# Kernel tuning notes

Measured on AMD Instinct MI355X. Metric: run time of the kernel, lower is better.

The kernel has to match this reference:

```python
import jax, jax.numpy as jnp
import numpy as np

N = 50000   # nodes
E = 100000  # directed edges
G = 2048    # graphs in batch
D = 32      # hidden dim
F_NODE = 11
F_EDGE = 4


def setup_inputs() -> dict:
    key = jax.random.key(0)
    ks = jax.random.split(key, 12)
    s = 0.1
    return {
        "x": jax.random.normal(ks[0], (N, F_NODE), dtype=jnp.float32),
        "edge_attr": jax.random.uniform(ks[1], (E, F_EDGE), dtype=jnp.float32),
        "lin0_w": jax.random.normal(ks[2], (D, F_NODE), dtype=jnp.float32) * s,
        "lin0_b": jnp.zeros((D,), jnp.float32),
        "nn_w": jax.random.normal(ks[3], (D * D, F_EDGE), dtype=jnp.float32) * s,
        "nn_b": jnp.zeros((D * D,), jnp.float32),
        "root_w": jax.random.normal(ks[4], (D, D), dtype=jnp.float32) * s,
        "conv_b": jnp.zeros((D,), jnp.float32),
        "gru_wi": jax.random.normal(ks[5], (3 * D, D), dtype=jnp.float32) * s,
        "gru_wh": jax.random.normal(ks[6], (3 * D, D), dtype=jnp.float32) * s,
        "gru_bi": jnp.zeros((3 * D,), jnp.float32),
        "gru_bh": jnp.zeros((3 * D,), jnp.float32),
        "lin1_w": jax.random.normal(ks[7], (2, D), dtype=jnp.float32) * s,
        "lin1_b": jnp.zeros((2,), jnp.float32),
        "edge_index": jax.random.randint(ks[8], (2, E), 0, N, dtype=jnp.int32),
        "batch": jnp.sort(jax.random.randint(ks[9], (N,), 0, G, dtype=jnp.int32)),
    }


def _gru_step(m, h, wi, wh, bi, bh):
    # single-step torch.nn.GRU cell math
    gi = m @ wi.T + bi            # [N, 3D]
    gh = h @ wh.T + bh            # [N, 3D]
    ir, iz, inn = jnp.split(gi, 3, axis=-1)
    hr, hz, hn = jnp.split(gh, 3, axis=-1)
    r = jax.nn.sigmoid(ir + hr)
    z = jax.nn.sigmoid(iz + hz)
    n = jnp.tanh(inn + r * hn)
    return (1.0 - z) * n + z * h


def reference(x, edge_attr, lin0_w, lin0_b, nn_w, nn_b, root_w, conv_b,
              gru_wi, gru_wh, gru_bi, gru_bh, lin1_w, lin1_b,
              edge_index, batch):
    src, dst = edge_index[0], edge_index[1]
    out = jax.nn.relu(x @ lin0_w.T + lin0_b)   # [N, D]
    h = out
    # per-edge 32x32 weight from edge MLP (edge_attr fixed -> hoisted out of loop)
    W_e = (edge_attr @ nn_w.T + nn_b).reshape(E, D, D)
    for _ in range(3):
        msg = jnp.einsum('ei,eio->eo', out[src], W_e)                  # [E, D]
        aggr = jax.ops.segment_sum(msg, dst, num_segments=N)           # add-aggregate
        m = jax.nn.relu(aggr + out @ root_w + conv_b)                  # NNConv root + bias
        h = _gru_step(m, h, gru_wi, gru_wh, gru_bi, gru_bh)
        out = h
    cnt = jax.ops.segment_sum(jnp.ones((N,), x.dtype), batch, num_segments=G)
    pooled = jax.ops.segment_sum(out, batch, num_segments=G) / jnp.maximum(cnt, 1.0)[:, None]
    logits = pooled @ lin1_w.T + lin1_b                                # [G, 2]
    return jax.nn.log_softmax(logits, axis=1)
```

## Files before the change

### kernel.cpp

```cpp
#include <hip/hip_runtime.h>
#include <hip/hip_bf16.h>

#define NN 50000
#define EE 100000
#define GG 2048
#define NB2 391

typedef float v2f __attribute__((ext_vector_type(2)));
__device__ __forceinline__ v2f fma2(v2f a, float b, v2f c) {
    return __builtin_elementwise_fma(a, (v2f){b, b}, c);
}

__device__ __forceinline__ float b2f(unsigned short u) {
    union { unsigned int i; float f; } x; x.i = (unsigned int)u << 16; return x.f;
}
__device__ __forceinline__ unsigned short f2b(float f) {
    union { float f; unsigned int i; } x; x.f = f;
    unsigned int b = x.i + (0x7FFFu + ((x.i >> 16) & 1u));
    return (unsigned short)(b >> 16);
}

__global__ __launch_bounds__(256) void k_setup(
    const float* __restrict__ x, const float* __restrict__ lw,
    const float* __restrict__ lb, const float* __restrict__ nnw,
    const float* __restrict__ nnb, const float* __restrict__ rootw,
    const float* __restrict__ wi, const float* __restrict__ wh,
    const int* __restrict__ ei, float* __restrict__ feat,
    float* __restrict__ Wre, float4* __restrict__ rw4,
    float4* __restrict__ wi4, int* __restrict__ cnt) {
    int blk = blockIdx.x;
    int t = threadIdx.x;
    if (blk < 6250) {
        int idx = blk * 256 + t;
        if (idx >= NN * 32) return;
        int n = idx >> 5, o = idx & 31;
        const float* xr = x + n * 11;
        const float* wr = lw + o * 11;
        float acc = lb[o];
#pragma unroll
        for (int i = 0; i < 11; ++i) acc += xr[i] * wr[i];
        feat[idx] = fmaxf(acc, 0.f);
    } else if (blk < 6278) {
        int idx = (blk - 6250) * 256 + t;
        if (idx < 5120) {
            int c = idx >> 5, i = idx & 31;
            float v;
            if (c < 128) v = nnw[((i << 5) + (c & 31)) * 4 + (c >> 5)];
            else         v = nnb[(i << 5) + (c - 128)];
            Wre[idx] = v;
        } else if (idx < 6144) {
            int j = idx - 5120;
            int k = j >> 5, o = j & 31;
            rw4[j] = make_float4(rootw[k * 32 + o], wh[o * 32 + k],
                                 wh[(32 + o) * 32 + k], wh[(64 + o) * 32 + k]);
        } else if (idx < 7168) {
            int j = idx - 6144;
            int k = j >> 5, o = j & 31;
            wi4[j] = make_float4(wi[o * 32 + k], wi[(32 + o) * 32 + k],
                                 wi[(64 + o) * 32 + k], 0.f);
        }
    } else {
        int e = (blk - 6278) * 256 + t;
        if (e >= EE) return;
        atomicAdd(&cnt[ei[EE + e]], 1);
        atomicAdd(&cnt[NN + ei[e]], 1);
    }
}

__global__ __launch_bounds__(256) void k_scan1(const int* __restrict__ cnt,
                                               int* __restrict__ tmp,
                                               int* __restrict__ bsum) {
    __shared__ int sd[256];
    int t = threadIdx.x;
    int i = blockIdx.x * 256 + t;
    int v = (i < 2 * NN) ? cnt[i] : 0;
    sd[t] = v;
    __syncthreads();
#pragma unroll
    for (int off = 1; off < 256; off <<= 1) {
        int x = (t >= off) ? sd[t - off] : 0;
        __syncthreads();
        sd[t] += x;
        __syncthreads();
    }
    if (i < 2 * NN) tmp[i] = sd[t];
    if (t == 255) bsum[blockIdx.x] = sd[255];
}

__global__ __launch_bounds__(512) void k_scan2(int* __restrict__ bsum) {
    __shared__ int sd[512];
    int t = threadIdx.x;
    int v = (t < NB2) ? bsum[t] : 0;
    sd[t] = v;
    __syncthreads();
#pragma unroll
    for (int off = 1; off < 512; off <<= 1) {
        int x = (t >= off) ? sd[t - off] : 0;
        __syncthreads();
        sd[t] += x;
        __syncthreads();
    }
    if (t < NB2) bsum[t] = sd[t];
}

__global__ void k_scan3(const int* __restrict__ cnt, const int* __restrict__ tmp,
                        const int* __restrict__ bsum, int* __restrict__ row_ptr,
                        int* __restrict__ cursor, int* __restrict__ out_ptr,
                        int* __restrict__ cursor2) {
    int i = blockIdx.x * blockDim.x + threadIdx.x;
    if (i >= 2 * NN) return;
    int base = (blockIdx.x > 0) ? bsum[blockIdx.x - 1] : 0;
    int excl = base + tmp[i] - cnt[i];
    if (i < NN) {
        row_ptr[i] = excl;
        cursor[i] = excl;
        if (i == 0) row_ptr[NN] = EE;
    } else {
        int j = i - NN;
        out_ptr[j] = excl - EE;
        cursor2[j] = excl - EE;
        if (j == 0) out_ptr[NN] = EE;
    }
}

__global__ __launch_bounds__(256) void k_scatter_y(
    const int* __restrict__ ei, const float* __restrict__ ea,
    int* __restrict__ cursor, int* __restrict__ cursor2,
    int* __restrict__ esrc, float4* __restrict__ eea,
    int* __restrict__ oslot, float4* __restrict__ oea,
    const float* __restrict__ feat, const float* __restrict__ Wre,
    unsigned short* __restrict__ yb) {
    int blk = blockIdx.x;
    if (blk < 391) {
        int e = blk * 256 + threadIdx.x;
        if (e >= EE) return;
        int s = ei[e], d = ei[EE + e];
        float4 a = make_float4(ea[e * 4 + 0], ea[e * 4 + 1], ea[e * 4 + 2], ea[e * 4 + 3]);
        int slot = atomicAdd(&cursor[d], 1);
        esrc[slot] = s;
        eea[slot] = a;
        int pos = atomicAdd(&cursor2[s], 1);
        oslot[pos] = slot;
        oea[pos] = a;
        return;
    }
    int by = blk - 391;
    int bx = by % 782, q = by / 782;
    int lane = threadIdx.x & 63;
    int wv = __builtin_amdgcn_readfirstlane(threadIdx.x >> 6);
    int n = bx * 64 + lane;
    if (n >= NN) return;
    int c0 = q * 40 + wv * 10;
    float fr[32];
    const float4* f4 = (const float4*)(feat + (long)n * 32);
#pragma unroll
    for (int qq = 0; qq < 8; ++qq) {
        float4 v = f4[qq];
        fr[4 * qq + 0] = v.x; fr[4 * qq + 1] = v.y;
        fr[4 * qq + 2] = v.z; fr[4 * qq + 3] = v.w;
    }
    float acc[10];
#pragma unroll
    for (int cc = 0; cc < 10; ++cc) {
        const float* w = Wre + (c0 + cc) * 32;
        float a = 0.f;
#pragma unroll
        for (int i = 0; i < 32; ++i) a += fr[i] * w[i];
        acc[cc] = a;
    }
    unsigned short* yr = yb + (long)n * 160 + c0;
#pragma unroll
    for (int qq = 0; qq < 5; ++qq) {
        unsigned int wlo = f2b(acc[2 * qq]);
        unsigned int whi = f2b(acc[2 * qq + 1]);
        ((unsigned int*)yr)[qq] = wlo | (whi << 16);
    }
}

__global__ __launch_bounds__(256) void k_msg(
    const unsigned short* __restrict__ yb, const int* __restrict__ esrc,
    const float4* __restrict__ eea, float* __restrict__ msg) {
    int idx = blockIdx.x * 256 + threadIdx.x;
    if (idx >= EE * 32) return;
    int slot = idx >> 5, o = idx & 31;
    int s = esrc[slot];
    float4 a = eea[slot];
    const unsigned short* yr = yb + (long)s * 160;
    float y0 = b2f(yr[o]);
    float y1 = b2f(yr[32 + o]);
    float y2 = b2f(yr[64 + o]);
    float y3 = b2f(yr[96 + o]);
    float y4 = b2f(yr[128 + o]);
    msg[idx] = y4 + a.x * y0 + a.y * y1 + a.z * y2 + a.w * y3;
}

__global__ __launch_bounds__(256) void k_conv_update(
    const float* __restrict__ msg_in, const int* __restrict__ row_ptr,
    const float4* __restrict__ rw4, const float* __restrict__ convb,
    const float4* __restrict__ wi4, const float* __restrict__ bi,
    const float* __restrict__ bh, const float4* __restrict__ nnw4,
    const float* __restrict__ nnb, const int* __restrict__ out_ptr,
    const int* __restrict__ oslot, const float4* __restrict__ oea,
    float* __restrict__ feat, float* __restrict__ msg_out, int write_msg) {
    __shared__ float fsT[32][36];
    __shared__ float msT[32][36];
    int t = threadIdx.x;
    int g = t >> 5, o = t & 31;
    int gc = g * 4;
    int nb = blockIdx.x * 32 + gc;
    float f[4], m[4];
    float cb = convb[o];
#pragma unroll
    for (int j = 0; j < 4; ++j) {
        int n = nb + j;
        bool v = (n < NN);
        f[j] = v ? feat[n * 32 + o] : 0.f;
        m[j] = cb;
        if (v) {
            int e0 = row_ptr[n], e1 = row_ptr[n + 1];
            for (int e = e0; e < e1; ++e)
                m[j] += msg_in[(e << 5) + o];
        }
    }
    *(float4*)&fsT[o][gc] = make_float4(f[0], f[1], f[2], f[3]);
    __syncthreads();

    float bhr = bh[o], bhz = bh[32 + o], bhn = bh[64 + o];
    v2f m01 = {m[0], m[1]}, m23 = {m[2], m[3]};
    v2f ghr01 = {bhr, bhr}, ghr23 = {bhr, bhr};
    v2f ghz01 = {bhz, bhz}, ghz23 = {bhz, bhz};
    v2f ghn01 = {bhn, bhn}, ghn23 = {bhn, bhn};
#pragma unroll 4
    for (int i = 0; i < 32; ++i) {
        float4 w = rw4[i * 32 + o];
        float4 fv = *(const float4*)&fsT[i][gc];
        v2f f01 = {fv.x, fv.y}, f23 = {fv.z, fv.w};
        m01 = fma2(f01, w.x, m01);   m23 = fma2(f23, w.x, m23);
        ghr01 = fma2(f01, w.y, ghr01); ghr23 = fma2(f23, w.y, ghr23);
        ghz01 = fma2(f01, w.z, ghz01); ghz23 = fma2(f23, w.z, ghz23);
        ghn01 = fma2(f01, w.w, ghn01); ghn23 = fma2(f23, w.w, ghn23);
    }
    float mm0 = fmaxf(m01.x, 0.f), mm1 = fmaxf(m01.y, 0.f);
    float mm2 = fmaxf(m23.x, 0.f), mm3 = fmaxf(m23.y, 0.f);
    *(float4*)&msT[o][gc] = make_float4(mm0, mm1, mm2, mm3);
    __syncthreads();

    float bir = bi[o], biz = bi[32 + o], bin_ = bi[64 + o];
    v2f gir01 = {bir, bir}, gir23 = {bir, bir};
    v2f giz01 = {biz, biz}, giz23 = {biz, biz};
    v2f gin01 = {bin_, bin_}, gin23 = {bin_, bin_};
#pragma unroll 4
    for (int k = 0; k < 32; ++k) {
        float4 w = wi4[k * 32 + o];
        float4 mv = *(const float4*)&msT[k][gc];
        v2f p01 = {mv.x, mv.y}, p23 = {mv.z, mv.w};
        gir01 = fma2(p01, w.x, gir01); gir23 = fma2(p23, w.x, gir23);
        giz01 = fma2(p01, w.y, giz01); giz23 = fma2(p23, w.y, giz23);
        gin01 = fma2(p01, w.z, gin01); gin23 = fma2(p23, w.z, gin23);
    }
    float girA[4] = {gir01.x, gir01.y, gir23.x, gir23.y};
    float gizA[4] = {giz01.x, giz01.y, giz23.x, giz23.y};
    float ginA[4] = {gin01.x, gin01.y, gin23.x, gin23.y};
    float ghrA[4] = {ghr01.x, ghr01.y, ghr23.x, ghr23.y};
    float ghzA[4] = {ghz01.x, ghz01.y, ghz23.x, ghz23.y};
    float ghnA[4] = {ghn01.x, ghn01.y, ghn23.x, ghn23.y};
    float fn[4];
#pragma unroll
    for (int j = 0; j < 4; ++j) {
        int n = nb + j;
        float r = 1.f / (1.f + __expf(-(girA[j] + ghrA[j])));
        float z = 1.f / (1.f + __expf(-(gizA[j] + ghzA[j])));
        float nt = tanhf(ginA[j] + r * ghnA[j]);
        fn[j] = (1.f - z) * nt + z * f[j];
        if (n < NN) feat[n * 32 + o] = fn[j];
    }
    if (!write_msg) return;

    *(float4*)&fsT[o][gc] = make_float4(fn[0], fn[1], fn[2], fn[3]);
    v2f y0_01 = {0.f, 0.f}, y0_23 = {0.f, 0.f};
    v2f y1_01 = {0.f, 0.f}, y1_23 = {0.f, 0.f};
    v2f y2_01 = {0.f, 0.f}, y2_23 = {0.f, 0.f};
    v2f y3_01 = {0.f, 0.f}, y3_23 = {0.f, 0.f};
    v2f y4_01 = {0.f, 0.f}, y4_23 = {0.f, 0.f};
#pragma unroll 4
    for (int i = 0; i < 32; ++i) {
        float4 w = nnw4[i * 32 + o];
        float w1 = nnb[i * 32 + o];
        float4 fv = *(const float4*)&fsT[i][gc];
        v2f f01 = {fv.x, fv.y}, f23 = {fv.z, fv.w};
        y0_01 = fma2(f01, w.x, y0_01); y0_23 = fma2(f23, w.x, y0_23);
        y1_01 = fma2(f01, w.y, y1_01); y1_23 = fma2(f23, w.y, y1_23);
        y2_01 = fma2(f01, w.z, y2_01); y2_23 = fma2(f23, w.z, y2_23);
        y3_01 = fma2(f01, w.w, y3_01); y3_23 = fma2(f23, w.w, y3_23);
        y4_01 = fma2(f01, w1, y4_01);  y4_23 = fma2(f23, w1, y4_23);
    }
    float ya0[4] = {y0_01.x, y0_01.y, y0_23.x, y0_23.y};
    float ya1[4] = {y1_01.x, y1_01.y, y1_23.x, y1_23.y};
    float ya2[4] = {y2_01.x, y2_01.y, y2_23.x, y2_23.y};
    float ya3[4] = {y3_01.x, y3_01.y, y3_23.x, y3_23.y};
    float ya4[4] = {y4_01.x, y4_01.y, y4_23.x, y4_23.y};
#pragma unroll
    for (int j = 0; j < 4; ++j) {
        int n = nb + j;
        if (n < NN) {
            int p0 = out_ptr[n], p1 = out_ptr[n + 1];
            for (int p = p0; p < p1; ++p) {
                float4 a = oea[p];
                int slot = oslot[p];
                msg_out[(slot << 5) + o] =
                    ya4[j] + a.x * ya0[j] + a.y * ya1[j]
                           + a.z * ya2[j] + a.w * ya3[j];
            }
        }
    }
}

__global__ __launch_bounds__(64) void k_pool_final(
    const float* __restrict__ feat, const int* __restrict__ batch,
    const float* __restrict__ w, const float* __restrict__ b,
    float* __restrict__ out) {
    int g = blockIdx.x;
    int t = threadIdx.x;
    int o = t & 31, h = t >> 5;
    int lo = 0, hi = NN;
    while (lo < hi) { int mid = (lo + hi) >> 1; if (batch[mid] < g) lo = mid + 1; else hi = mid; }
    int start = lo;
    hi = NN;
    while (lo < hi) { int mid = (lo + hi) >> 1; if (batch[mid] <= g) lo = mid + 1; else hi = mid; }
    int end = lo;
    float acc = 0.f;
    for (int n = start + h; n < end; n += 2) acc += feat[(long)n * 32 + o];
    acc += __shfl_xor(acc, 32, 64);
    float p = acc / fmaxf((float)(end - start), 1.f);
    float l0 = p * w[o], l1 = p * w[32 + o];
#pragma unroll
    for (int s = 16; s >= 1; s >>= 1) {
        l0 += __shfl_xor(l0, s, 64);
        l1 += __shfl_xor(l1, s, 64);
    }
    if (t == 0) {
        l0 += b[0]; l1 += b[1];
        float mx = fmaxf(l0, l1);
        float lse = mx + logf(__expf(l0 - mx) + __expf(l1 - mx));
        out[g * 2 + 0] = l0 - lse;
        out[g * 2 + 1] = l1 - lse;
    }
}

extern "C" void kernel_launch(void* const* d_in, const int* in_sizes, int n_in,
                              void* d_out, int out_size, void* d_ws, size_t ws_size,
                              hipStream_t stream) {
    const float* x        = (const float*)d_in[0];
    const float* edge_attr= (const float*)d_in[1];
    const float* lin0_w   = (const float*)d_in[2];
    const float* lin0_b   = (const float*)d_in[3];
    const float* nn_w     = (const float*)d_in[4];
    const float* nn_b     = (const float*)d_in[5];
    const float* root_w   = (const float*)d_in[6];
    const float* conv_b   = (const float*)d_in[7];
    const float* gru_wi   = (const float*)d_in[8];
    const float* gru_wh   = (const float*)d_in[9];
    const float* gru_bi   = (const float*)d_in[10];
    const float* gru_bh   = (const float*)d_in[11];
    const float* lin1_w   = (const float*)d_in[12];
    const float* lin1_b   = (const float*)d_in[13];
    const int*   edge_idx = (const int*)d_in[14];
    const int*   batch    = (const int*)d_in[15];
    float* out = (float*)d_out;

    float4* rw4   = (float4*)d_ws;
    float4* wi4   = rw4 + 1024;
    float4* eea   = wi4 + 1024;
    float4* oea   = eea + EE;
    float*  feat  = (float*)(oea + EE);
    float*  Wre   = feat + (long)NN * 32;
    int*    cnt   = (int*)(Wre + 5120);
    int*    tmp   = cnt + 2 * NN;
    int*    bsum  = tmp + 2 * NN;
    int*    row_ptr = bsum + 512;
    int*    cursor  = row_ptr + NN + 1;
    int*    out_ptr = cursor + NN;
    int*    cursor2 = out_ptr + NN + 1;
    int*    esrc  = cursor2 + NN;
    int*    oslot = esrc + EE;
    unsigned short* yb = (unsigned short*)(oslot + EE);
    float*  msgA  = (float*)(yb + (long)NN * 160);
    float*  msgB  = msgA + (long)EE * 32;
    const float4* nnw4 = (const float4*)nn_w;

    hipMemsetAsync(cnt, 0, 2 * NN * sizeof(int), stream);

    k_setup<<<6250 + 28 + 391, 256, 0, stream>>>(x, lin0_w, lin0_b, nn_w, nn_b,
                                                 root_w, gru_wi, gru_wh, edge_idx,
                                                 feat, Wre, rw4, wi4, cnt);

    k_scan1<<<NB2, 256, 0, stream>>>(cnt, tmp, bsum);
    k_scan2<<<1, 512, 0, stream>>>(bsum);
    k_scan3<<<NB2, 256, 0, stream>>>(cnt, tmp, bsum, row_ptr, cursor, out_ptr, cursor2);

    k_scatter_y<<<391 + 782 * 4, 256, 0, stream>>>(edge_idx, edge_attr, cursor, cursor2,
                                                   esrc, eea, oslot, oea, feat, Wre, yb);
    k_msg<<<(EE * 32 + 255) / 256, 256, 0, stream>>>(yb, esrc, eea, msgA);

    k_conv_update<<<(NN + 31) / 32, 256, 0, stream>>>(msgA, row_ptr, rw4, conv_b, wi4,
                                                      gru_bi, gru_bh, nnw4, nn_b,
                                                      out_ptr, oslot, oea,
                                                      feat, msgB, 1);
    k_conv_update<<<(NN + 31) / 32, 256, 0, stream>>>(msgB, row_ptr, rw4, conv_b, wi4,
                                                      gru_bi, gru_bh, nnw4, nn_b,
                                                      out_ptr, oslot, oea,
                                                      feat, msgA, 1);
    k_conv_update<<<(NN + 31) / 32, 256, 0, stream>>>(msgA, row_ptr, rw4, conv_b, wi4,
                                                      gru_bi, gru_bh, nnw4, nn_b,
                                                      out_ptr, oslot, oea,
                                                      feat, msgB, 0);

    k_pool_final<<<GG, 64, 0, stream>>>(feat, batch, lin1_w, lin1_b, out);
}
```

Measured before the change: 273.4 us.

## Fuse first-layer message gather into conv update and store messages as bf16

```diff
diff --git a/kernel.cpp b/kernel.cpp
--- a/kernel.cpp
+++ b/kernel.cpp
@@ -177,31 +177,17 @@
     }
 }
 
-__global__ __launch_bounds__(256) void k_msg(
-    const unsigned short* __restrict__ yb, const int* __restrict__ esrc,
-    const float4* __restrict__ eea, float* __restrict__ msg) {
-    int idx = blockIdx.x * 256 + threadIdx.x;
-    if (idx >= EE * 32) return;
-    int slot = idx >> 5, o = idx & 31;
-    int s = esrc[slot];
-    float4 a = eea[slot];
-    const unsigned short* yr = yb + (long)s * 160;
-    float y0 = b2f(yr[o]);
-    float y1 = b2f(yr[32 + o]);
-    float y2 = b2f(yr[64 + o]);
-    float y3 = b2f(yr[96 + o]);
-    float y4 = b2f(yr[128 + o]);
-    msg[idx] = y4 + a.x * y0 + a.y * y1 + a.z * y2 + a.w * y3;
-}
-
 __global__ __launch_bounds__(256) void k_conv_update(
-    const float* __restrict__ msg_in, const int* __restrict__ row_ptr,
+    const unsigned short* __restrict__ msg_in, const int* __restrict__ row_ptr,
     const float4* __restrict__ rw4, const float* __restrict__ convb,
     const float4* __restrict__ wi4, const float* __restrict__ bi,
     const float* __restrict__ bh, const float4* __restrict__ nnw4,
     const float* __restrict__ nnb, const int* __restrict__ out_ptr,
     const int* __restrict__ oslot, const float4* __restrict__ oea,
-    float* __restrict__ feat, float* __restrict__ msg_out, int write_msg) {
+    const unsigned short* __restrict__ yb, const int* __restrict__ esrc,
+    const float4* __restrict__ eea,
+    float* __restrict__ feat, unsigned short* __restrict__ msg_out,
+    int gather_from_y, int write_msg) {
     __shared__ float fsT[32][36];
     __shared__ float msT[32][36];
     int t = threadIdx.x;
@@ -218,8 +204,22 @@
         m[j] = cb;
         if (v) {
             int e0 = row_ptr[n], e1 = row_ptr[n + 1];
-            for (int e = e0; e < e1; ++e)
-                m[j] += msg_in[(e << 5) + o];
+            if (gather_from_y) {
+                for (int e = e0; e < e1; ++e) {
+                    int s = esrc[e];
+                    float4 a = eea[e];
+                    const unsigned short* yr = yb + (long)s * 160;
+                    float y0 = b2f(yr[o]);
+                    float y1 = b2f(yr[32 + o]);
+                    float y2 = b2f(yr[64 + o]);
+                    float y3 = b2f(yr[96 + o]);
+                    float y4 = b2f(yr[128 + o]);
+                    m[j] += y4 + a.x * y0 + a.y * y1 + a.z * y2 + a.w * y3;
+                }
+            } else {
+                for (int e = e0; e < e1; ++e)
+                    m[j] += b2f(msg_in[(e << 5) + o]);
+            }
         }
     }
     *(float4*)&fsT[o][gc] = make_float4(f[0], f[1], f[2], f[3]);
@@ -308,8 +308,8 @@
                 float4 a = oea[p];
                 int slot = oslot[p];
                 msg_out[(slot << 5) + o] =
-                    ya4[j] + a.x * ya0[j] + a.y * ya1[j]
-                           + a.z * ya2[j] + a.w * ya3[j];
+                    f2b(ya4[j] + a.x * ya0[j] + a.y * ya1[j]
+                               + a.z * ya2[j] + a.w * ya3[j]);
             }
         }
     }
@@ -383,9 +383,9 @@
     int*    cursor2 = out_ptr + NN + 1;
     int*    esrc  = cursor2 + NN;
     int*    oslot = esrc + EE;
-    unsigned short* yb = (unsigned short*)(oslot + EE);
-    float*  msgA  = (float*)(yb + (long)NN * 160);
-    float*  msgB  = msgA + (long)EE * 32;
+    unsigned short* yb   = (unsigned short*)(oslot + EE);
+    unsigned short* msgA = yb + (long)NN * 160;
+    unsigned short* msgB = msgA + (long)EE * 32;
     const float4* nnw4 = (const float4*)nn_w;
 
     hipMemsetAsync(cnt, 0, 2 * NN * sizeof(int), stream);
@@ -400,20 +400,22 @@
 
     k_scatter_y<<<391 + 782 * 4, 256, 0, stream>>>(edge_idx, edge_attr, cursor, cursor2,
                                                    esrc, eea, oslot, oea, feat, Wre, yb);
-    k_msg<<<(EE * 32 + 255) / 256, 256, 0, stream>>>(yb, esrc, eea, msgA);
 
     k_conv_update<<<(NN + 31) / 32, 256, 0, stream>>>(msgA, row_ptr, rw4, conv_b, wi4,
                                                       gru_bi, gru_bh, nnw4, nn_b,
                                                       out_ptr, oslot, oea,
-                                                      feat, msgB, 1);
+                                                      yb, esrc, eea,
+                                                      feat, msgB, 1, 1);
     k_conv_update<<<(NN + 31) / 32, 256, 0, stream>>>(msgB, row_ptr, rw4, conv_b, wi4,
                                                       gru_bi, gru_bh, nnw4, nn_b,
                                                       out_ptr, oslot, oea,
-                                                      feat, msgA, 1);
+                                                      yb, esrc, eea,
+                                                      feat, msgA, 0, 1);
     k_conv_update<<<(NN + 31) / 32, 256, 0, stream>>>(msgA, row_ptr, rw4, conv_b, wi4,
                                                       gru_bi, gru_bh, nnw4, nn_b,
                                                       out_ptr, oslot, oea,
-                                                      feat, msgB, 0);
+                                                      yb, esrc, eea,
+                                                      feat, msgB, 0, 0);
 
     k_pool_final<<<GG, 64, 0, stream>>>(feat, batch, lin1_w, lin1_b, out);
 }
```

New measurement: 266.4 us. 2.6% less time.

## Merge preprocessing into one cooperative kernel with grid syncs and push-style first messages

Applied to the files above, without the earlier changes.

```diff
diff --git a/kernel.cpp b/kernel.cpp
--- a/kernel.cpp
+++ b/kernel.cpp
@@ -1,200 +1,180 @@
 #include <hip/hip_runtime.h>
+#include <hip/hip_cooperative_groups.h>
 #include <hip/hip_bf16.h>
+
+namespace cg = cooperative_groups;
 
 #define NN 50000
 #define EE 100000
 #define GG 2048
-#define NB2 391
+#define GRD 512
+#define BLK 512
+#define CH  196
 
 typedef float v2f __attribute__((ext_vector_type(2)));
 __device__ __forceinline__ v2f fma2(v2f a, float b, v2f c) {
     return __builtin_elementwise_fma(a, (v2f){b, b}, c);
 }
 
-__device__ __forceinline__ float b2f(unsigned short u) {
-    union { unsigned int i; float f; } x; x.i = (unsigned int)u << 16; return x.f;
-}
-__device__ __forceinline__ unsigned short f2b(float f) {
-    union { float f; unsigned int i; } x; x.f = f;
-    unsigned int b = x.i + (0x7FFFu + ((x.i >> 16) & 1u));
-    return (unsigned short)(b >> 16);
-}
-
-__global__ __launch_bounds__(256) void k_setup(
-    const float* __restrict__ x, const float* __restrict__ lw,
-    const float* __restrict__ lb, const float* __restrict__ nnw,
-    const float* __restrict__ nnb, const float* __restrict__ rootw,
-    const float* __restrict__ wi, const float* __restrict__ wh,
-    const int* __restrict__ ei, float* __restrict__ feat,
-    float* __restrict__ Wre, float4* __restrict__ rw4,
-    float4* __restrict__ wi4, int* __restrict__ cnt) {
-    int blk = blockIdx.x;
+struct ProArgs {
+    const float *x, *lw, *lb, *nnb, *rootw, *wi, *wh, *ea;
+    const float4 *nnw4;
+    const int *ei;
+    float *feat;
+    float4 *rw4, *wi4;
+    int *cnt, *tmp, *bsum, *row_ptr, *cursor, *out_ptr, *cursor2, *oslot;
+    float4 *oea;
+    float *msgA;
+};
+
+__global__ __launch_bounds__(512, 4) void k_pro(ProArgs a) {
+    cg::grid_group grid = cg::this_grid();
+    __shared__ __align__(16) int sd[512];
+    __shared__ __align__(16) float fsT[32][68];
     int t = threadIdx.x;
-    if (blk < 6250) {
-        int idx = blk * 256 + t;
-        if (idx >= NN * 32) return;
-        int n = idx >> 5, o = idx & 31;
-        const float* xr = x + n * 11;
-        const float* wr = lw + o * 11;
-        float acc = lb[o];
-#pragma unroll
-        for (int i = 0; i < 11; ++i) acc += xr[i] * wr[i];
-        feat[idx] = fmaxf(acc, 0.f);
-    } else if (blk < 6278) {
-        int idx = (blk - 6250) * 256 + t;
-        if (idx < 5120) {
-            int c = idx >> 5, i = idx & 31;
-            float v;
-            if (c < 128) v = nnw[((i << 5) + (c & 31)) * 4 + (c >> 5)];
-            else         v = nnb[(i << 5) + (c - 128)];
-            Wre[idx] = v;
-        } else if (idx < 6144) {
-            int j = idx - 5120;
+    int gid = blockIdx.x * BLK + t;
+    const int gstr = GRD * BLK;
+
+    for (int i = gid; i < 2 * NN; i += gstr) a.cnt[i] = 0;
+    for (int i = gid; i < NN * 32; i += gstr) {
+        int n = i >> 5, o = i & 31;
+        const float* xr = a.x + n * 11;
+        const float* wr = a.lw + o * 11;
+        float acc = a.lb[o];
+#pragma unroll
+        for (int k = 0; k < 11; ++k) acc += xr[k] * wr[k];
+        a.feat[i] = fmaxf(acc, 0.f);
+    }
+    if (gid < 2048) {
+        if (gid < 1024) {
+            int k = gid >> 5, o = gid & 31;
+            a.rw4[gid] = make_float4(a.rootw[k * 32 + o], a.wh[o * 32 + k],
+                                     a.wh[(32 + o) * 32 + k], a.wh[(64 + o) * 32 + k]);
+        } else {
+            int j = gid - 1024;
             int k = j >> 5, o = j & 31;
-            rw4[j] = make_float4(rootw[k * 32 + o], wh[o * 32 + k],
-                                 wh[(32 + o) * 32 + k], wh[(64 + o) * 32 + k]);
-        } else if (idx < 7168) {
-            int j = idx - 6144;
-            int k = j >> 5, o = j & 31;
-            wi4[j] = make_float4(wi[o * 32 + k], wi[(32 + o) * 32 + k],
-                                 wi[(64 + o) * 32 + k], 0.f);
-        }
-    } else {
-        int e = (blk - 6278) * 256 + t;
-        if (e >= EE) return;
-        atomicAdd(&cnt[ei[EE + e]], 1);
-        atomicAdd(&cnt[NN + ei[e]], 1);
-    }
-}
-
-__global__ __launch_bounds__(256) void k_scan1(const int* __restrict__ cnt,
-                                               int* __restrict__ tmp,
-                                               int* __restrict__ bsum) {
-    __shared__ int sd[256];
-    int t = threadIdx.x;
-    int i = blockIdx.x * 256 + t;
-    int v = (i < 2 * NN) ? cnt[i] : 0;
-    sd[t] = v;
-    __syncthreads();
-#pragma unroll
-    for (int off = 1; off < 256; off <<= 1) {
-        int x = (t >= off) ? sd[t - off] : 0;
+            a.wi4[j] = make_float4(a.wi[o * 32 + k], a.wi[(32 + o) * 32 + k],
+                                   a.wi[(64 + o) * 32 + k], 0.f);
+        }
+    }
+    grid.sync();
+
+    for (int e = gid; e < EE; e += gstr) {
+        atomicAdd(&a.cnt[a.ei[EE + e]], 1);
+        atomicAdd(&a.cnt[NN + a.ei[e]], 1);
+    }
+    grid.sync();
+
+    if (blockIdx.x < CH) {
+        int i = blockIdx.x * 512 + t;
+        int v = (i < 2 * NN) ? a.cnt[i] : 0;
+        sd[t] = v;
         __syncthreads();
-        sd[t] += x;
+#pragma unroll
+        for (int off = 1; off < 512; off <<= 1) {
+            int xz = (t >= off) ? sd[t - off] : 0;
+            __syncthreads();
+            sd[t] += xz;
+            __syncthreads();
+        }
+        if (i < 2 * NN) a.tmp[i] = sd[t];
+        if (t == 511) a.bsum[blockIdx.x] = sd[511];
+    }
+    grid.sync();
+
+    if (blockIdx.x == 0) {
+        int v = (t < CH) ? a.bsum[t] : 0;
+        sd[t] = v;
         __syncthreads();
-    }
-    if (i < 2 * NN) tmp[i] = sd[t];
-    if (t == 255) bsum[blockIdx.x] = sd[255];
-}
-
-__global__ __launch_bounds__(512) void k_scan2(int* __restrict__ bsum) {
-    __shared__ int sd[512];
-    int t = threadIdx.x;
-    int v = (t < NB2) ? bsum[t] : 0;
-    sd[t] = v;
-    __syncthreads();
-#pragma unroll
-    for (int off = 1; off < 512; off <<= 1) {
-        int x = (t >= off) ? sd[t - off] : 0;
+#pragma unroll
+        for (int off = 1; off < 512; off <<= 1) {
+            int xz = (t >= off) ? sd[t - off] : 0;
+            __syncthreads();
+            sd[t] += xz;
+            __syncthreads();
+        }
+        if (t < CH) a.bsum[t] = sd[t];
+    }
+    grid.sync();
+
+    for (int i = gid; i < 2 * NN; i += gstr) {
+        int c = i >> 9;
+        int base = c ? a.bsum[c - 1] : 0;
+        int excl = base + a.tmp[i] - a.cnt[i];
+        if (i < NN) {
+            a.row_ptr[i] = excl;
+            a.cursor[i] = excl;
+            if (i == 0) a.row_ptr[NN] = EE;
+        } else {
+            int j = i - NN;
+            a.out_ptr[j] = excl - EE;
+            a.cursor2[j] = excl - EE;
+            if (j == 0) a.out_ptr[NN] = EE;
+        }
+    }
+    grid.sync();
+
+    for (int e = gid; e < EE; e += gstr) {
+        int s = a.ei[e], d = a.ei[EE + e];
+        int slot = atomicAdd(&a.cursor[d], 1);
+        int pos = atomicAdd(&a.cursor2[s], 1);
+        a.oslot[pos] = slot;
+        a.oea[pos] = make_float4(a.ea[e * 4 + 0], a.ea[e * 4 + 1],
+                                 a.ea[e * 4 + 2], a.ea[e * 4 + 3]);
+    }
+    grid.sync();
+
+    int g = t >> 5, o = t & 31;
+    for (int nb0 = (int)blockIdx.x * 64; nb0 < NN; nb0 += GRD * 64) {
+        int nb = nb0 + g * 4;
+        float f0 = (nb < NN) ? a.feat[(nb) * 32 + o] : 0.f;
+        float f1 = (nb + 1 < NN) ? a.feat[(nb + 1) * 32 + o] : 0.f;
+        float f2 = (nb + 2 < NN) ? a.feat[(nb + 2) * 32 + o] : 0.f;
+        float f3 = (nb + 3 < NN) ? a.feat[(nb + 3) * 32 + o] : 0.f;
+        *(float4*)&fsT[o][g * 4] = make_float4(f0, f1, f2, f3);
         __syncthreads();
-        sd[t] += x;
+        v2f y0a[2], y1a[2], y2a[2], y3a[2], y4a[2];
+#pragma unroll
+        for (int h = 0; h < 2; ++h) {
+            y0a[h] = (v2f){0.f, 0.f}; y1a[h] = (v2f){0.f, 0.f};
+            y2a[h] = (v2f){0.f, 0.f}; y3a[h] = (v2f){0.f, 0.f};
+            y4a[h] = (v2f){0.f, 0.f};
+        }
+#pragma unroll 2
+        for (int i = 0; i < 32; ++i) {
+            float4 w = a.nnw4[i * 32 + o];
+            float w1 = a.nnb[i * 32 + o];
+            float4 fv = *(const float4*)&fsT[i][g * 4];
+            v2f fA = {fv.x, fv.y}, fB = {fv.z, fv.w};
+            y0a[0] = fma2(fA, w.x, y0a[0]); y0a[1] = fma2(fB, w.x, y0a[1]);
+            y1a[0] = fma2(fA, w.y, y1a[0]); y1a[1] = fma2(fB, w.y, y1a[1]);
+            y2a[0] = fma2(fA, w.z, y2a[0]); y2a[1] = fma2(fB, w.z, y2a[1]);
+            y3a[0] = fma2(fA, w.w, y3a[0]); y3a[1] = fma2(fB, w.w, y3a[1]);
+            y4a[0] = fma2(fA, w1, y4a[0]);  y4a[1] = fma2(fB, w1, y4a[1]);
+        }
+        float ya0[4] = {y0a[0].x, y0a[0].y, y0a[1].x, y0a[1].y};
+        float ya1[4] = {y1a[0].x, y1a[0].y, y1a[1].x, y1a[1].y};
+        float ya2[4] = {y2a[0].x, y2a[0].y, y2a[1].x, y2a[1].y};
+        float ya3[4] = {y3a[0].x, y3a[0].y, y3a[1].x, y3a[1].y};
+        float ya4[4] = {y4a[0].x, y4a[0].y, y4a[1].x, y4a[1].y};
+#pragma unroll
+        for (int j = 0; j < 4; ++j) {
+            int n = nb + j;
+            if (n < NN) {
+                int p0 = a.out_ptr[n], p1 = a.out_ptr[n + 1];
+                for (int p = p0; p < p1; ++p) {
+                    float4 aa = a.oea[p];
+                    a.msgA[(a.oslot[p] << 5) + o] =
+                        ya4[j] + aa.x * ya0[j] + aa.y * ya1[j]
+                               + aa.z * ya2[j] + aa.w * ya3[j];
+                }
+            }
+        }
         __syncthreads();
     }
-    if (t < NB2) bsum[t] = sd[t];
-}
-
-__global__ void k_scan3(const int* __restrict__ cnt, const int* __restrict__ tmp,
-                        const int* __restrict__ bsum, int* __restrict__ row_ptr,
-                        int* __restrict__ cursor, int* __restrict__ out_ptr,
-                        int* __restrict__ cursor2) {
-    int i = blockIdx.x * blockDim.x + threadIdx.x;
-    if (i >= 2 * NN) return;
-    int base = (blockIdx.x > 0) ? bsum[blockIdx.x - 1] : 0;
-    int excl = base + tmp[i] - cnt[i];
-    if (i < NN) {
-        row_ptr[i] = excl;
-        cursor[i] = excl;
-        if (i == 0) row_ptr[NN] = EE;
-    } else {
-        int j = i - NN;
-        out_ptr[j] = excl - EE;
-        cursor2[j] = excl - EE;
-        if (j == 0) out_ptr[NN] = EE;
-    }
-}
-
-__global__ __launch_bounds__(256) void k_scatter_y(
-    const int* __restrict__ ei, const float* __restrict__ ea,
-    int* __restrict__ cursor, int* __restrict__ cursor2,
-    int* __restrict__ esrc, float4* __restrict__ eea,
-    int* __restrict__ oslot, float4* __restrict__ oea,
-    const float* __restrict__ feat, const float* __restrict__ Wre,
-    unsigned short* __restrict__ yb) {
-    int blk = blockIdx.x;
-    if (blk < 391) {
-        int e = blk * 256 + threadIdx.x;
-        if (e >= EE) return;
-        int s = ei[e], d = ei[EE + e];
-        float4 a = make_float4(ea[e * 4 + 0], ea[e * 4 + 1], ea[e * 4 + 2], ea[e * 4 + 3]);
-        int slot = atomicAdd(&cursor[d], 1);
-        esrc[slot] = s;
-        eea[slot] = a;
-        int pos = atomicAdd(&cursor2[s], 1);
-        oslot[pos] = slot;
-        oea[pos] = a;
-        return;
-    }
-    int by = blk - 391;
-    int bx = by % 782, q = by / 782;
-    int lane = threadIdx.x & 63;
-    int wv = __builtin_amdgcn_readfirstlane(threadIdx.x >> 6);
-    int n = bx * 64 + lane;
-    if (n >= NN) return;
-    int c0 = q * 40 + wv * 10;
-    float fr[32];
-    const float4* f4 = (const float4*)(feat + (long)n * 32);
-#pragma unroll
-    for (int qq = 0; qq < 8; ++qq) {
-        float4 v = f4[qq];
-        fr[4 * qq + 0] = v.x; fr[4 * qq + 1] = v.y;
-        fr[4 * qq + 2] = v.z; fr[4 * qq + 3] = v.w;
-    }
-    float acc[10];
-#pragma unroll
-    for (int cc = 0; cc < 10; ++cc) {
-        const float* w = Wre + (c0 + cc) * 32;
-        float a = 0.f;
-#pragma unroll
-        for (int i = 0; i < 32; ++i) a += fr[i] * w[i];
-        acc[cc] = a;
-    }
-    unsigned short* yr = yb + (long)n * 160 + c0;
-#pragma unroll
-    for (int qq = 0; qq < 5; ++qq) {
-        unsigned int wlo = f2b(acc[2 * qq]);
-        unsigned int whi = f2b(acc[2 * qq + 1]);
-        ((unsigned int*)yr)[qq] = wlo | (whi << 16);
-    }
-}
-
-__global__ __launch_bounds__(256) void k_msg(
-    const unsigned short* __restrict__ yb, const int* __restrict__ esrc,
-    const float4* __restrict__ eea, float* __restrict__ msg) {
-    int idx = blockIdx.x * 256 + threadIdx.x;
-    if (idx >= EE * 32) return;
-    int slot = idx >> 5, o = idx & 31;
-    int s = esrc[slot];
-    float4 a = eea[slot];
-    const unsigned short* yr = yb + (long)s * 160;
-    float y0 = b2f(yr[o]);
-    float y1 = b2f(yr[32 + o]);
-    float y2 = b2f(yr[64 + o]);
-    float y3 = b2f(yr[96 + o]);
-    float y4 = b2f(yr[128 + o]);
-    msg[idx] = y4 + a.x * y0 + a.y * y1 + a.z * y2 + a.w * y3;
-}
-
-__global__ __launch_bounds__(256) void k_conv_update(
+}
+
+__global__ __launch_bounds__(256) void k_conv(
     const float* __restrict__ msg_in, const int* __restrict__ row_ptr,
     const float4* __restrict__ rw4, const float* __restrict__ convb,
     const float4* __restrict__ wi4, const float* __restrict__ bi,
@@ -202,8 +182,8 @@
     const float* __restrict__ nnb, const int* __restrict__ out_ptr,
     const int* __restrict__ oslot, const float4* __restrict__ oea,
     float* __restrict__ feat, float* __restrict__ msg_out, int write_msg) {
-    __shared__ float fsT[32][36];
-    __shared__ float msT[32][36];
+    __shared__ __align__(16) float fsT[32][36];
+    __shared__ __align__(16) float msT[32][36];
     int t = threadIdx.x;
     int g = t >> 5, o = t & 31;
     int gc = g * 4;
@@ -230,7 +210,7 @@
     v2f ghr01 = {bhr, bhr}, ghr23 = {bhr, bhr};
     v2f ghz01 = {bhz, bhz}, ghz23 = {bhz, bhz};
     v2f ghn01 = {bhn, bhn}, ghn23 = {bhn, bhn};
-#pragma unroll 4
+#pragma unroll 2
     for (int i = 0; i < 32; ++i) {
         float4 w = rw4[i * 32 + o];
         float4 fv = *(const float4*)&fsT[i][gc];
@@ -249,7 +229,7 @@
     v2f gir01 = {bir, bir}, gir23 = {bir, bir};
     v2f giz01 = {biz, biz}, giz23 = {biz, biz};
     v2f gin01 = {bin_, bin_}, gin23 = {bin_, bin_};
-#pragma unroll 4
+#pragma unroll 2
     for (int k = 0; k < 32; ++k) {
         float4 w = wi4[k * 32 + o];
         float4 mv = *(const float4*)&msT[k][gc];
@@ -282,7 +262,7 @@
     v2f y2_01 = {0.f, 0.f}, y2_23 = {0.f, 0.f};
     v2f y3_01 = {0.f, 0.f}, y3_23 = {0.f, 0.f};
     v2f y4_01 = {0.f, 0.f}, y4_23 = {0.f, 0.f};
-#pragma unroll 4
+#pragma unroll 2
     for (int i = 0; i < 32; ++i) {
         float4 w = nnw4[i * 32 + o];
         float w1 = nnb[i * 32 + o];
@@ -370,50 +350,42 @@
 
     float4* rw4   = (float4*)d_ws;
     float4* wi4   = rw4 + 1024;
-    float4* eea   = wi4 + 1024;
-    float4* oea   = eea + EE;
+    float4* oea   = wi4 + 1024;
     float*  feat  = (float*)(oea + EE);
-    float*  Wre   = feat + (long)NN * 32;
-    int*    cnt   = (int*)(Wre + 5120);
+    int*    cnt   = (int*)(feat + (long)NN * 32);
     int*    tmp   = cnt + 2 * NN;
     int*    bsum  = tmp + 2 * NN;
     int*    row_ptr = bsum + 512;
     int*    cursor  = row_ptr + NN + 1;
     int*    out_ptr = cursor + NN;
     int*    cursor2 = out_ptr + NN + 1;
-    int*    esrc  = cursor2 + NN;
-    int*    oslot = esrc + EE;
-    unsigned short* yb = (unsigned short*)(oslot + EE);
-    float*  msgA  = (float*)(yb + (long)NN * 160);
+    int*    oslot = cursor2 + NN;
+    float*  msgA  = (float*)(oslot + EE);
     float*  msgB  = msgA + (long)EE * 32;
     const float4* nnw4 = (const float4*)nn_w;
 
-    hipMemsetAsync(cnt, 0, 2 * NN * sizeof(int), stream);
-
-    k_setup<<<6250 + 28 + 391, 256, 0, stream>>>(x, lin0_w, lin0_b, nn_w, nn_b,
-                                                 root_w, gru_wi, gru_wh, edge_idx,
-                                                 feat, Wre, rw4, wi4, cnt);
-
-    k_scan1<<<NB2, 256, 0, stream>>>(cnt, tmp, bsum);
-    k_scan2<<<1, 512, 0, stream>>>(bsum);
-    k_scan3<<<NB2, 256, 0, stream>>>(cnt, tmp, bsum, row_ptr, cursor, out_ptr, cursor2);
-
-    k_scatter_y<<<391 + 782 * 4, 256, 0, stream>>>(edge_idx, edge_attr, cursor, cursor2,
-                                                   esrc, eea, oslot, oea, feat, Wre, yb);
-    k_msg<<<(EE * 32 + 255) / 256, 256, 0, stream>>>(yb, esrc, eea, msgA);
-
-    k_conv_update<<<(NN + 31) / 32, 256, 0, stream>>>(msgA, row_ptr, rw4, conv_b, wi4,
-                                                      gru_bi, gru_bh, nnw4, nn_b,
-                                                      out_ptr, oslot, oea,
-                                                      feat, msgB, 1);
-    k_conv_update<<<(NN + 31) / 32, 256, 0, stream>>>(msgB, row_ptr, rw4, conv_b, wi4,
-                                                      gru_bi, gru_bh, nnw4, nn_b,
-                                                      out_ptr, oslot, oea,
-                                                      feat, msgA, 1);
-    k_conv_update<<<(NN + 31) / 32, 256, 0, stream>>>(msgA, row_ptr, rw4, conv_b, wi4,
-                                                      gru_bi, gru_bh, nnw4, nn_b,
-                                                      out_ptr, oslot, oea,
-                                                      feat, msgB, 0);
+    ProArgs pa;
+    pa.x = x; pa.lw = lin0_w; pa.lb = lin0_b; pa.nnb = nn_b;
+    pa.rootw = root_w; pa.wi = gru_wi; pa.wh = gru_wh; pa.ea = edge_attr;
+    pa.nnw4 = nnw4; pa.ei = edge_idx;
+    pa.feat = feat; pa.rw4 = rw4; pa.wi4 = wi4;
+    pa.cnt = cnt; pa.tmp = tmp; pa.bsum = bsum;
+    pa.row_ptr = row_ptr; pa.cursor = cursor;
+    pa.out_ptr = out_ptr; pa.cursor2 = cursor2;
+    pa.oslot = oslot; pa.oea = oea; pa.msgA = msgA;
+    void* pargs[] = { &pa };
+    hipLaunchCooperativeKernel(reinterpret_cast<void*>(&k_pro),
+                               dim3(GRD), dim3(BLK), pargs, 0, stream);
+
+    k_conv<<<(NN + 31) / 32, 256, 0, stream>>>(
+        msgA, row_ptr, rw4, conv_b, wi4, gru_bi, gru_bh, nnw4, nn_b,
+        out_ptr, oslot, oea, feat, msgB, 1);
+    k_conv<<<(NN + 31) / 32, 256, 0, stream>>>(
+        msgB, row_ptr, rw4, conv_b, wi4, gru_bi, gru_bh, nnw4, nn_b,
+        out_ptr, oslot, oea, feat, msgA, 1);
+    k_conv<<<(NN + 31) / 32, 256, 0, stream>>>(
+        msgA, row_ptr, rw4, conv_b, wi4, gru_bi, gru_bh, nnw4, nn_b,
+        out_ptr, oslot, oea, feat, msgB, 0);
 
     k_pool_final<<<GG, 64, 0, stream>>>(feat, batch, lin1_w, lin1_b, out);
 }
```

New measurement: 628.5 us. 130% more time.
